# Optimization experiments

Measured on AMD Instinct MI355X. Metric: run time of the kernel, lower is better.

The kernel has to match this reference:

```python
import jax, jax.numpy as jnp
import numpy as np

D_MODEL, FFN, N_EXP = 1024, 4096, 8
BS, L = 4, 2048


def setup_inputs() -> dict:
    key = jax.random.key(0)
    ks = jax.random.split(key, 7)
    s = 0.02
    return {
        "x": jax.random.normal(ks[0], (BS, L, D_MODEL), dtype=jnp.float32),
        "gate_w": s * jax.random.normal(ks[1], (D_MODEL, N_EXP), dtype=jnp.float32),
        "gate_b": jnp.zeros((N_EXP,), dtype=jnp.float32),
        "W1": s * jax.random.normal(ks[2], (N_EXP, D_MODEL, FFN), dtype=jnp.float32),
        "b1": jnp.zeros((N_EXP, FFN), dtype=jnp.float32),
        "W2": s * jax.random.normal(ks[3], (N_EXP, FFN, D_MODEL), dtype=jnp.float32),
        "b2": jnp.zeros((N_EXP, D_MODEL), dtype=jnp.float32),
    }


def reference(x, gate_w, gate_b, W1, b1, W2, b2):
    # gate logits [bs, l, E]; NOTE: original applies Softmax(dim=1) -> over seq dim
    logits = jnp.einsum("bld,de->ble", x, gate_w) + gate_b
    probs = jax.nn.softmax(logits, axis=1)  # faithful to nn.Softmax(dim=1)
    idx = jnp.argmax(probs, axis=-1)  # top-1 expert per token, [bs, l]
    # topk_weights are computed in the original but never applied to output.
    out = jnp.zeros_like(x)
    for e in range(N_EXP):  # fixed small expert loop (structurally distinct weights)
        h = jax.nn.gelu(jnp.einsum("bld,df->blf", x, W1[e]) + b1[e], approximate=False)
        y = jnp.einsum("blf,fd->bld", h, W2[e]) + b2[e]
        out = out + jnp.where((idx == e)[..., None], y, jnp.float32(0.0))
    return out
```

## Files before the change

### kernel.cpp

```cpp
#include <hip/hip_runtime.h>
#include <hip/hip_bf16.h>

typedef unsigned short u16;
typedef unsigned int u32;

using bf16x8 = __attribute__((ext_vector_type(8))) short;
using f32x4  = __attribute__((ext_vector_type(4))) float;

static constexpr int TOK  = 8192;
static constexpr int SEQ  = 2048;
static constexpr int DM   = 1024;
static constexpr int FF   = 4096;
static constexpr int NE   = 8;
static constexpr int MAXT = 72;
static constexpr int KS2  = 4;
static constexpr int NWG1 = MAXT * (FF/128);
static constexpr int NWG2 = MAXT * (DM/128) * KS2;

static constexpr size_t O_LOGITS = 0;
static constexpr size_t O_M      = 262144;
static constexpr size_t O_Z      = O_M + 128;
static constexpr size_t O_CNT    = O_Z + 128;
static constexpr size_t O_CUR    = O_CNT + 64;
static constexpr size_t O_OFF    = O_CUR + 64;
static constexpr size_t O_DESC   = 263168;
static constexpr size_t O_PERM   = 266240;
static constexpr size_t O_IDX    = 299008;
static constexpr size_t O_XG     = 524288;
static constexpr size_t O_W1T    = O_XG  + (size_t)TOK*DM*2;
static constexpr size_t O_W2T    = O_W1T + (size_t)NE*DM*FF*2;
static constexpr size_t O_H      = O_W2T + (size_t)NE*DM*FF*2;

__device__ __forceinline__ u16 f2bf(float f){
  __hip_bfloat16 h = __float2bfloat16(f);
  return *reinterpret_cast<u16*>(&h);
}

__device__ __forceinline__ void gld_lds16(const void* g, void* l){
  __builtin_amdgcn_global_load_lds((const __attribute__((address_space(1))) void*)g,
                                   (__attribute__((address_space(3))) void*)l, 16, 0, 0);
}

__device__ __forceinline__ float gelu_f(float v){
  float u = v * fmaf(v*v, 0.044715f, 1.0f) * 0.7978845608f;
  float ex = __builtin_amdgcn_exp2f(u * -2.885390082f);
  return v * __builtin_amdgcn_rcpf(1.0f + ex);
}

__global__ void k_gate(const float* __restrict__ x, const float* __restrict__ gw,
                       const float* __restrict__ gb, float* __restrict__ logits){
  __shared__ float sgw[NE*DM];
  for (int i = threadIdx.x; i < DM*NE; i += 256){
    int d = i >> 3, e = i & 7;
    sgw[e*DM + d] = gw[i];
  }
  __syncthreads();
  int wave = threadIdx.x >> 6, lane = threadIdx.x & 63;
  int t = blockIdx.x * 4 + wave;
  const float4* xr = (const float4*)(x + (size_t)t * DM);
  float acc[NE];
#pragma unroll
  for (int e = 0; e < NE; ++e) acc[e] = 0.f;
#pragma unroll
  for (int k = 0; k < 4; ++k){
    int v4 = k*64 + lane;
    float4 v = xr[v4];
#pragma unroll
    for (int e = 0; e < NE; ++e){
      const float4 g = *(const float4*)&sgw[e*DM + v4*4];
      acc[e] = fmaf(v.x, g.x, fmaf(v.y, g.y, fmaf(v.z, g.z, fmaf(v.w, g.w, acc[e]))));
    }
  }
#pragma unroll
  for (int off = 32; off; off >>= 1)
#pragma unroll
    for (int e = 0; e < NE; ++e) acc[e] += __shfl_xor(acc[e], off);
  if (lane == 0){
#pragma unroll
    for (int e = 0; e < NE; ++e) logits[(size_t)t*NE + e] = acc[e] + gb[e];
  }
}

__global__ void k_lse(const float* __restrict__ logits, float* __restrict__ mOut,
                      float* __restrict__ zOut){
  int be = blockIdx.x;
  int b = be >> 3, e = be & 7;
  const float* base = logits + ((size_t)b*SEQ)*NE + e;
  float m = -INFINITY;
  for (int l = threadIdx.x; l < SEQ; l += 256) m = fmaxf(m, base[(size_t)l*NE]);
  __shared__ float red[8];
#pragma unroll
  for (int off = 32; off; off >>= 1) m = fmaxf(m, __shfl_xor(m, off));
  if ((threadIdx.x & 63) == 0) red[threadIdx.x >> 6] = m;
  __syncthreads();
  m = fmaxf(fmaxf(red[0], red[1]), fmaxf(red[2], red[3]));
  float s = 0.f;
  for (int l = threadIdx.x; l < SEQ; l += 256) s += expf(base[(size_t)l*NE] - m);
#pragma unroll
  for (int off = 32; off; off >>= 1) s += __shfl_xor(s, off);
  if ((threadIdx.x & 63) == 0) red[4 + (threadIdx.x >> 6)] = s;
  __syncthreads();
  if (threadIdx.x == 0){ mOut[be] = m; zOut[be] = red[4]+red[5]+red[6]+red[7]; }
}

__global__ void k_route(const float* __restrict__ logits, const float* __restrict__ m,
                        const float* __restrict__ z, u32* __restrict__ cnt,
                        int* __restrict__ idx){
  int t = blockIdx.x*256 + threadIdx.x;
  int b = t >> 11;
  const float* lr = logits + (size_t)t*NE;
  float best = -INFINITY; int be = 0;
#pragma unroll
  for (int e = 0; e < NE; ++e){
    float p = expf(lr[e] - m[b*NE + e]) / z[b*NE + e];
    if (p > best){ best = p; be = e; }
  }
  idx[t] = be;
  atomicAdd(&cnt[be], 1u);
}

__global__ void k_plan(const u32* __restrict__ cnt, int* __restrict__ off,
                       int4* __restrict__ desc, u32* __restrict__ cur){
  if (threadIdx.x == 0){
    int offs[NE+1]; int o = 0;
    for (int e = 0; e < NE; ++e){ offs[e] = o; o += (int)cnt[e]; }
    offs[NE] = o;
    int nt = 0;
    for (int e = 0; e < NE; ++e){
      int c = (int)cnt[e];
      for (int s = 0; s < c; s += 128)
        desc[nt++] = make_int4(e, offs[e] + s, min(128, c - s), 0);
      off[e] = offs[e]; cur[e] = 0u;
    }
    off[NE] = offs[NE];
    for (int i = nt; i < MAXT; ++i) desc[i] = make_int4(-1, 0, 0, 0);
  }
}

__global__ void k_scatter(const int* __restrict__ idx, const int* __restrict__ off,
                          u32* __restrict__ cur, int* __restrict__ perm){
  int t = blockIdx.x*256 + threadIdx.x;
  int e = idx[t];
  int pos = off[e] + (int)atomicAdd(&cur[e], 1u);
  perm[pos] = t;
}

__global__ void k_gather(const float* __restrict__ x, const int* __restrict__ perm,
                         const int* __restrict__ idx, const float* __restrict__ b2,
                         u16* __restrict__ Xg, float* __restrict__ out){
  int p = blockIdx.x;
  int t = perm[p];
  int e = idx[t];
  const float4* src = (const float4*)(x + (size_t)t*DM);
  float4 v = src[threadIdx.x];
  uint2 o;
  o.x = (u32)f2bf(v.x) | ((u32)f2bf(v.y) << 16);
  o.y = (u32)f2bf(v.z) | ((u32)f2bf(v.w) << 16);
  *(uint2*)(Xg + (size_t)p*DM + threadIdx.x*4) = o;
  float4 bv = ((const float4*)(b2 + (size_t)e*DM))[threadIdx.x];
  ((float4*)(out + (size_t)t*DM))[threadIdx.x] = bv;
}

__global__ void k_trans(const float* __restrict__ in, u16* __restrict__ out,
                        int R, int C){
  __shared__ float tile[64][65];
  int e = blockIdx.z;
  int r0 = blockIdx.x*64, c0 = blockIdx.y*64;
  const float* src = in + ((size_t)e*R + r0)*C + c0;
  int lr = threadIdx.x >> 4, lc = (threadIdx.x & 15) * 4;
#pragma unroll
  for (int i = 0; i < 4; ++i){
    float4 v = *(const float4*)(src + (size_t)(lr + i*16)*C + lc);
    tile[lr + i*16][lc+0] = v.x; tile[lr + i*16][lc+1] = v.y;
    tile[lr + i*16][lc+2] = v.z; tile[lr + i*16][lc+3] = v.w;
  }
  __syncthreads();
  u16* dst = out + ((size_t)e*C + c0)*R + r0;
  int rr = (threadIdx.x & 7) * 8;
  int ocb = threadIdx.x >> 3;
#pragma unroll
  for (int p = 0; p < 2; ++p){
    int oc = ocb + p*32;
    u16 w[8];
#pragma unroll
    for (int k = 0; k < 8; ++k) w[k] = f2bf(tile[rr + k][oc]);
    uint4 o;
    o.x = (u32)w[0] | ((u32)w[1] << 16);
    o.y = (u32)w[2] | ((u32)w[3] << 16);
    o.z = (u32)w[4] | ((u32)w[5] << 16);
    o.w = (u32)w[6] | ((u32)w[7] << 16);
    *(uint4*)(dst + (size_t)oc*R + rr) = o;
  }
}


__global__ __launch_bounds__(512) void k_ffn1(const u16* __restrict__ Xg,
    const u16* __restrict__ W1T, const float* __restrict__ b1,
    u16* __restrict__ H, const int4* __restrict__ desc){
  int pid = blockIdx.x;
  int pid_sw = (pid & 7) * (NWG1/8) + (pid >> 3);
  int ng  = pid_sw / (MAXT*8);
  int rem = pid_sw - ng*(MAXT*8);
  int mt  = rem >> 3;
  int n0  = (ng*8 + (rem & 7)) * 128;
  int4 dd = desc[mt];
  int e = dd.x; if (e < 0) return;
  int m0 = dd.y, valid = dd.z;
  __shared__ __align__(16) u16 lA[2][128*32];
  __shared__ __align__(16) u16 lB[2][128*32];
  int tid = threadIdx.x, lane = tid & 63, wave = tid >> 6;
  int wr = wave >> 1, wc = wave & 1;
  const u16* Bsrc = W1T + ((size_t)e*FF + n0)*DM;
  f32x4 acc[2][4] = {};

  int srow = tid >> 2;
  int scol = (tid & 3) * 8;
  auto stage = [&](int buf, int kt){
    int k0 = kt * 32;
    int ra = m0 + srow; if (ra > TOK-1) ra = TOK-1;
    gld_lds16(Xg   + (size_t)ra  *DM + k0 + scol, &lA[buf][tid*8]);
    gld_lds16(Bsrc + (size_t)srow*DM + k0 + scol, &lB[buf][tid*8]);
  };

  stage(0, 0);
  __syncthreads();
  const int KT = DM / 32;
  for (int kt = 0; kt < KT; ++kt){
    int cur = kt & 1;
    if (kt + 1 < KT) stage(cur ^ 1, kt + 1);
    const u16* pa = &lA[cur][(wr*32 + (lane & 15))*32 + (lane >> 4)*8];
    const u16* pb = &lB[cur][(wc*64 + (lane & 15))*32 + (lane >> 4)*8];
    bf16x8 a[2], b[4];
#pragma unroll
    for (int m = 0; m < 2; ++m) a[m] = *(const bf16x8*)(pa + m*16*32);
#pragma unroll
    for (int n = 0; n < 4; ++n) b[n] = *(const bf16x8*)(pb + n*16*32);
#pragma unroll
    for (int m = 0; m < 2; ++m)
#pragma unroll
      for (int n = 0; n < 4; ++n)
        acc[m][n] = __builtin_amdgcn_mfma_f32_16x16x32_bf16(a[m], b[n], acc[m][n], 0, 0, 0);
    __syncthreads();
  }

#pragma unroll
  for (int n = 0; n < 4; ++n){
    int col = n0 + wc*64 + n*16 + (lane & 15);
    float bias = b1[(size_t)e*FF + col];
#pragma unroll
    for (int m = 0; m < 2; ++m){
      int rbase = wr*32 + m*16 + ((lane >> 4) << 2);
#pragma unroll
      for (int j = 0; j < 4; ++j){
        int rit = rbase + j;
        if (rit < valid){
          float v = acc[m][n][j] + bias;
          H[(size_t)(m0 + rit)*FF + col] = f2bf(gelu_f(v));
        }
      }
    }
  }
}

__global__ __launch_bounds__(512) void k_ffn2(const u16* __restrict__ H,
    const u16* __restrict__ W2T, float* __restrict__ out,
    const int4* __restrict__ desc, const int* __restrict__ perm){
  int pid = blockIdx.x;
  int pid_sw = (pid & 7) * (NWG2/8) + (pid >> 3);
  int ks  = pid_sw / (MAXT*8);
  int rem = pid_sw - ks*(MAXT*8);
  int mt  = rem >> 3;
  int n0  = (rem & 7) * 128;
  int4 dd = desc[mt];
  int e = dd.x; if (e < 0) return;
  int m0 = dd.y, valid = dd.z;
  __shared__ __align__(16) u16 lA[2][128*32];
  __shared__ __align__(16) u16 lB[2][128*32];
  int tid = threadIdx.x, lane = tid & 63, wave = tid >> 6;
  int wr = wave >> 1, wc = wave & 1;
  const u16* Bsrc = W2T + ((size_t)e*DM + n0)*FF;
  const int kbase = ks * (FF/KS2);
  f32x4 acc[2][4] = {};

  int srow = tid >> 2;
  int scol = (tid & 3) * 8;
  auto stage = [&](int buf, int kt){
    int k0 = kbase + kt * 32;
    int ra = m0 + srow; if (ra > TOK-1) ra = TOK-1;
    gld_lds16(H    + (size_t)ra  *FF + k0 + scol, &lA[buf][tid*8]);
    gld_lds16(Bsrc + (size_t)srow*FF + k0 + scol, &lB[buf][tid*8]);
  };

  stage(0, 0);
  __syncthreads();
  const int KT = (FF/KS2) / 32;
  for (int kt = 0; kt < KT; ++kt){
    int cur = kt & 1;
    if (kt + 1 < KT) stage(cur ^ 1, kt + 1);
    const u16* pa = &lA[cur][(wr*32 + (lane & 15))*32 + (lane >> 4)*8];
    const u16* pb = &lB[cur][(wc*64 + (lane & 15))*32 + (lane >> 4)*8];
    bf16x8 a[2], b[4];
#pragma unroll
    for (int m = 0; m < 2; ++m) a[m] = *(const bf16x8*)(pa + m*16*32);
#pragma unroll
    for (int n = 0; n < 4; ++n) b[n] = *(const bf16x8*)(pb + n*16*32);
#pragma unroll
    for (int m = 0; m < 2; ++m)
#pragma unroll
      for (int n = 0; n < 4; ++n)
        acc[m][n] = __builtin_amdgcn_mfma_f32_16x16x32_bf16(a[m], b[n], acc[m][n], 0, 0, 0);
    __syncthreads();
  }

#pragma unroll
  for (int m = 0; m < 2; ++m){
#pragma unroll
    for (int j = 0; j < 4; ++j){
      int rit = wr*32 + m*16 + ((lane >> 4) << 2) + j;
      if (rit < valid){
        int tok = perm[m0 + rit];
#pragma unroll
        for (int n = 0; n < 4; ++n){
          int col = n0 + wc*64 + n*16 + (lane & 15);
          unsafeAtomicAdd(&out[(size_t)tok*DM + col], acc[m][n][j]);
        }
      }
    }
  }
}

extern "C" void kernel_launch(void* const* d_in, const int* in_sizes, int n_in,
                              void* d_out, int out_size, void* d_ws, size_t ws_size,
                              hipStream_t stream){
  const float* x   = (const float*)d_in[0];
  const float* gw  = (const float*)d_in[1];
  const float* gb  = (const float*)d_in[2];
  const float* W1  = (const float*)d_in[3];
  const float* b1  = (const float*)d_in[4];
  const float* W2  = (const float*)d_in[5];
  const float* b2  = (const float*)d_in[6];
  float* out = (float*)d_out;
  char* ws = (char*)d_ws;

  float* logits = (float*)(ws + O_LOGITS);
  float* mArr   = (float*)(ws + O_M);
  float* zArr   = (float*)(ws + O_Z);
  u32*   cnt    = (u32*)  (ws + O_CNT);
  u32*   cur    = (u32*)  (ws + O_CUR);
  int*   off    = (int*)  (ws + O_OFF);
  int4*  desc   = (int4*) (ws + O_DESC);
  int*   perm   = (int*)  (ws + O_PERM);
  int*   idx    = (int*)  (ws + O_IDX);
  u16*   Xg     = (u16*)  (ws + O_XG);
  u16*   W1T    = (u16*)  (ws + O_W1T);
  u16*   W2T    = (u16*)  (ws + O_W2T);
  u16*   Hbuf   = (u16*)  (ws + O_H);

  hipMemsetAsync(ws + O_CNT, 0, 128, stream);

  k_gate   <<<TOK/4, 256, 0, stream>>>(x, gw, gb, logits);
  k_lse    <<<32,    256, 0, stream>>>(logits, mArr, zArr);
  k_route  <<<TOK/256, 256, 0, stream>>>(logits, mArr, zArr, cnt, idx);
  k_plan   <<<1,     64,  0, stream>>>(cnt, off, desc, cur);
  k_scatter<<<TOK/256, 256, 0, stream>>>(idx, off, cur, perm);
  k_gather <<<TOK,   256, 0, stream>>>(x, perm, idx, b2, Xg, out);
  k_trans  <<<dim3(DM/64, FF/64, NE), 256, 0, stream>>>(W1, W1T, DM, FF);
  k_trans  <<<dim3(FF/64, DM/64, NE), 256, 0, stream>>>(W2, W2T, FF, DM);
  k_ffn1   <<<NWG1,  512, 0, stream>>>(Xg, W1T, b1, Hbuf, desc);
  k_ffn2   <<<NWG2,  512, 0, stream>>>(Hbuf, W2T, out, desc, perm);
}
```

Baseline: 482.9 us.

## Double K-tile depth to 64 and XOR-swizzle LDS layout in both FFN GEMMs

Both expert GEMM kernels now stage 64-wide K tiles instead of 32, which halves the number of barrier-separated iterations and doubles the MFMA work per sync. The LDS layout is XOR-swizzled on 16-byte slots by row, applied both when writing from global memory and when reading operands, so the ds_read_b128 fragment loads avoid bank conflicts. The cost is doubled LDS use (64 KB per block), which may lower occupancy.

```diff
diff --git a/kernel.cpp b/kernel.cpp
--- a/kernel.cpp
+++ b/kernel.cpp
@@ -206,40 +206,60 @@
   int4 dd = desc[mt];
   int e = dd.x; if (e < 0) return;
   int m0 = dd.y, valid = dd.z;
-  __shared__ __align__(16) u16 lA[2][128*32];
-  __shared__ __align__(16) u16 lB[2][128*32];
+  __shared__ __align__(16) u16 lA[2][128*64];
+  __shared__ __align__(16) u16 lB[2][128*64];
   int tid = threadIdx.x, lane = tid & 63, wave = tid >> 6;
   int wr = wave >> 1, wc = wave & 1;
   const u16* Bsrc = W1T + ((size_t)e*FF + n0)*DM;
   f32x4 acc[2][4] = {};
 
-  int srow = tid >> 2;
-  int scol = (tid & 3) * 8;
   auto stage = [&](int buf, int kt){
-    int k0 = kt * 32;
-    int ra = m0 + srow; if (ra > TOK-1) ra = TOK-1;
-    gld_lds16(Xg   + (size_t)ra  *DM + k0 + scol, &lA[buf][tid*8]);
-    gld_lds16(Bsrc + (size_t)srow*DM + k0 + scol, &lB[buf][tid*8]);
+    int k0 = kt * 64;
+#pragma unroll
+    for (int c = 0; c < 2; ++c){
+      int idx = tid + c*512;
+      int r = idx >> 3, s = idx & 7;
+      int sp = (s ^ (r & 7)) * 8;
+      int ra = m0 + r; if (ra > TOK-1) ra = TOK-1;
+      gld_lds16(Xg   + (size_t)ra*DM + k0 + sp, (char*)&lA[buf][0] + idx*16);
+      gld_lds16(Bsrc + (size_t)r *DM + k0 + sp, (char*)&lB[buf][0] + idx*16);
+    }
   };
 
   stage(0, 0);
   __syncthreads();
-  const int KT = DM / 32;
+  const int KT = DM / 64;
   for (int kt = 0; kt < KT; ++kt){
     int cur = kt & 1;
     if (kt + 1 < KT) stage(cur ^ 1, kt + 1);
-    const u16* pa = &lA[cur][(wr*32 + (lane & 15))*32 + (lane >> 4)*8];
-    const u16* pb = &lB[cur][(wc*64 + (lane & 15))*32 + (lane >> 4)*8];
-    bf16x8 a[2], b[4];
-#pragma unroll
-    for (int m = 0; m < 2; ++m) a[m] = *(const bf16x8*)(pa + m*16*32);
-#pragma unroll
-    for (int n = 0; n < 4; ++n) b[n] = *(const bf16x8*)(pb + n*16*32);
+    const char* cA = (const char*)&lA[cur][0];
+    const char* cB = (const char*)&lB[cur][0];
+    bf16x8 a[2][2], b[4][2];
+#pragma unroll
+    for (int m = 0; m < 2; ++m){
+      int R = wr*32 + m*16 + (lane & 15);
+#pragma unroll
+      for (int h = 0; h < 2; ++h){
+        int slot = (h*4 + (lane >> 4)) ^ (R & 7);
+        a[m][h] = *(const bf16x8*)(cA + R*128 + slot*16);
+      }
+    }
+#pragma unroll
+    for (int n = 0; n < 4; ++n){
+      int R = wc*64 + n*16 + (lane & 15);
+#pragma unroll
+      for (int h = 0; h < 2; ++h){
+        int slot = (h*4 + (lane >> 4)) ^ (R & 7);
+        b[n][h] = *(const bf16x8*)(cB + R*128 + slot*16);
+      }
+    }
 #pragma unroll
     for (int m = 0; m < 2; ++m)
 #pragma unroll
-      for (int n = 0; n < 4; ++n)
-        acc[m][n] = __builtin_amdgcn_mfma_f32_16x16x32_bf16(a[m], b[n], acc[m][n], 0, 0, 0);
+      for (int n = 0; n < 4; ++n){
+        acc[m][n] = __builtin_amdgcn_mfma_f32_16x16x32_bf16(a[m][0], b[n][0], acc[m][n], 0,0,0);
+        acc[m][n] = __builtin_amdgcn_mfma_f32_16x16x32_bf16(a[m][1], b[n][1], acc[m][n], 0,0,0);
+      }
     __syncthreads();
   }
 
@@ -274,41 +294,61 @@
   int4 dd = desc[mt];
   int e = dd.x; if (e < 0) return;
   int m0 = dd.y, valid = dd.z;
-  __shared__ __align__(16) u16 lA[2][128*32];
-  __shared__ __align__(16) u16 lB[2][128*32];
+  __shared__ __align__(16) u16 lA[2][128*64];
+  __shared__ __align__(16) u16 lB[2][128*64];
   int tid = threadIdx.x, lane = tid & 63, wave = tid >> 6;
   int wr = wave >> 1, wc = wave & 1;
   const u16* Bsrc = W2T + ((size_t)e*DM + n0)*FF;
   const int kbase = ks * (FF/KS2);
   f32x4 acc[2][4] = {};
 
-  int srow = tid >> 2;
-  int scol = (tid & 3) * 8;
   auto stage = [&](int buf, int kt){
-    int k0 = kbase + kt * 32;
-    int ra = m0 + srow; if (ra > TOK-1) ra = TOK-1;
-    gld_lds16(H    + (size_t)ra  *FF + k0 + scol, &lA[buf][tid*8]);
-    gld_lds16(Bsrc + (size_t)srow*FF + k0 + scol, &lB[buf][tid*8]);
+    int k0 = kbase + kt * 64;
+#pragma unroll
+    for (int c = 0; c < 2; ++c){
+      int idx = tid + c*512;
+      int r = idx >> 3, s = idx & 7;
+      int sp = (s ^ (r & 7)) * 8;
+      int ra = m0 + r; if (ra > TOK-1) ra = TOK-1;
+      gld_lds16(H    + (size_t)ra*FF + k0 + sp, (char*)&lA[buf][0] + idx*16);
+      gld_lds16(Bsrc + (size_t)r *FF + k0 + sp, (char*)&lB[buf][0] + idx*16);
+    }
   };
 
   stage(0, 0);
   __syncthreads();
-  const int KT = (FF/KS2) / 32;
+  const int KT = (FF/KS2) / 64;
   for (int kt = 0; kt < KT; ++kt){
     int cur = kt & 1;
     if (kt + 1 < KT) stage(cur ^ 1, kt + 1);
-    const u16* pa = &lA[cur][(wr*32 + (lane & 15))*32 + (lane >> 4)*8];
-    const u16* pb = &lB[cur][(wc*64 + (lane & 15))*32 + (lane >> 4)*8];
-    bf16x8 a[2], b[4];
-#pragma unroll
-    for (int m = 0; m < 2; ++m) a[m] = *(const bf16x8*)(pa + m*16*32);
-#pragma unroll
-    for (int n = 0; n < 4; ++n) b[n] = *(const bf16x8*)(pb + n*16*32);
+    const char* cA = (const char*)&lA[cur][0];
+    const char* cB = (const char*)&lB[cur][0];
+    bf16x8 a[2][2], b[4][2];
+#pragma unroll
+    for (int m = 0; m < 2; ++m){
+      int R = wr*32 + m*16 + (lane & 15);
+#pragma unroll
+      for (int h = 0; h < 2; ++h){
+        int slot = (h*4 + (lane >> 4)) ^ (R & 7);
+        a[m][h] = *(const bf16x8*)(cA + R*128 + slot*16);
+      }
+    }
+#pragma unroll
+    for (int n = 0; n < 4; ++n){
+      int R = wc*64 + n*16 + (lane & 15);
+#pragma unroll
+      for (int h = 0; h < 2; ++h){
+        int slot = (h*4 + (lane >> 4)) ^ (R & 7);
+        b[n][h] = *(const bf16x8*)(cB + R*128 + slot*16);
+      }
+    }
 #pragma unroll
     for (int m = 0; m < 2; ++m)
 #pragma unroll
-      for (int n = 0; n < 4; ++n)
-        acc[m][n] = __builtin_amdgcn_mfma_f32_16x16x32_bf16(a[m], b[n], acc[m][n], 0, 0, 0);
+      for (int n = 0; n < 4; ++n){
+        acc[m][n] = __builtin_amdgcn_mfma_f32_16x16x32_bf16(a[m][0], b[n][0], acc[m][n], 0,0,0);
+        acc[m][n] = __builtin_amdgcn_mfma_f32_16x16x32_bf16(a[m][1], b[n][1], acc[m][n], 0,0,0);
+      }
     __syncthreads();
   }
 
```

Result: no change. 490.5 us (+1.6%).
